# Performance work log

Hardware: AMD Instinct MI355X
Metric: run time of the kernel (lower is better)

Reference implementation:

```python
import jax, jax.numpy as jnp
import numpy as np
from jax import lax


def setup_inputs() -> dict:
    key = jax.random.key(0)
    B, N, R = 16, 4096, 256
    param = jax.random.normal(key, (B, N, R), dtype=jnp.float32)
    return {"param": param}


def reference(param) -> jnp.ndarray:
    # StiefelHouseholder.forward with is_thin=True (rank != n):
    #   v = tril(param, -1) + eye(n, rank)      -> unit-lower columns v_i
    #   tau_i = 2 / ||v_i||^2
    #   Q = (I - tau_1 v_1 v_1^T) ... (I - tau_R v_R v_R^T) @ I[:, :R]
    B, N, R = param.shape
    eye = jnp.eye(N, R, dtype=param.dtype)                      # [N, R]
    v = jnp.tril(param, k=-1) + eye[None]                       # [B, N, R]
    tau = 2.0 / jnp.sum(v * v, axis=1)                          # [B, R]

    Q0 = jnp.broadcast_to(eye, (B, N, R))                       # start from thin identity

    def body(Q, i):
        vi = v[:, :, i]                                          # [B, N]
        ti = tau[:, i]                                           # [B]
        w = jnp.einsum('bn,bnk->bk', vi, Q)                      # v_i^T Q
        Q = Q - (ti[:, None] * vi)[:, :, None] * w[:, None, :]   # rank-1 update
        return Q, None

    # Apply H_R first (rightmost factor), then H_{R-1}, ..., H_1.
    Q, _ = lax.scan(body, Q0, jnp.arange(R - 1, -1, -1))
    return Q                                                     # thin [B, N, R]
```

## Files before the change

kernel.cpp:

```cpp
#include <hip/hip_runtime.h>
#include <stdint.h>

#define B_ 16
#define N_ 4096
#define R_ 256

typedef short bf16x8 __attribute__((ext_vector_type(8)));
typedef float f32x4 __attribute__((ext_vector_type(4)));
typedef uint32_t u32;


__device__ __forceinline__ u32 pack_split(float x) {
  u32 u = __float_as_uint(x);
  u32 h = u & 0xffff0000u;
  float l = x - __uint_as_float(h);
  return h | (__float_as_uint(l) >> 16);
}

__device__ __forceinline__ void unpack8(const u32* w, bf16x8& hi, bf16x8& lo) {
  union { u32 u[4]; bf16x8 v; } H, L;
#pragma unroll
  for (int i = 0; i < 4; ++i) {
    u32 a = w[2 * i], b = w[2 * i + 1];
    H.u[i] = (a >> 16) | (b & 0xffff0000u);
    L.u[i] = (a & 0xffffu) | (b << 16);
  }
  hi = H.v; lo = L.v;
}

__device__ __forceinline__ void read_frag(const u32* rowbase, int row, int q2,
                                          bf16x8& hi, bf16x8& lo) {
  u32 w[8];
  const int s = row & 7;
  *(uint4*)&w[0] = *(const uint4*)(rowbase + (((q2    ) ^ s) << 2));
  *(uint4*)&w[4] = *(const uint4*)(rowbase + (((q2 + 1) ^ s) << 2));
  unpack8(w, hi, lo);
}

__device__ __forceinline__ void read_frag_f(const float* rowbase, int row, int q2,
                                            bf16x8& hi, bf16x8& lo) {
  float w[8];
  const int s = row & 7;
  *(float4*)&w[0] = *(const float4*)(rowbase + (((q2    ) ^ s) << 2));
  *(float4*)&w[4] = *(const float4*)(rowbase + (((q2 + 1) ^ s) << 2));
  union { u32 u[4]; bf16x8 v; } H, L;
#pragma unroll
  for (int i = 0; i < 4; ++i) {
    u32 a = __float_as_uint(w[2 * i]);
    u32 b = __float_as_uint(w[2 * i + 1]);
    u32 ah = a & 0xffff0000u, bh = b & 0xffff0000u;
    float la = w[2 * i]     - __uint_as_float(ah);
    float lb = w[2 * i + 1] - __uint_as_float(bh);
    H.u[i] = (a >> 16) | bh;
    L.u[i] = (__float_as_uint(la) >> 16) | (__float_as_uint(lb) & 0xffff0000u);
  }
  hi = H.v; lo = L.v;
}

__device__ __forceinline__ f32x4 mm3(bf16x8 ah, bf16x8 al, bf16x8 bh, bf16x8 bl,
                                     f32x4 c) {
  c = __builtin_amdgcn_mfma_f32_16x16x32_bf16(al, bh, c, 0, 0, 0);
  c = __builtin_amdgcn_mfma_f32_16x16x32_bf16(ah, bl, c, 0, 0, 0);
  c = __builtin_amdgcn_mfma_f32_16x16x32_bf16(ah, bh, c, 0, 0, 0);
  return c;
}

typedef __attribute__((address_space(1))) const u32* gas_p;
typedef __attribute__((address_space(3))) u32* las_p;
__device__ __forceinline__ void async_cp16(void* lds, const void* g) {
  __builtin_amdgcn_global_load_lds((gas_p)g, (las_p)lds, 16, 0, 0);
}

__global__ __launch_bounds__(256) void gram_kernel(const float* __restrict__ param,
                                                   float* __restrict__ SP) {
  const int tile = blockIdx.x, chunk = blockIdx.y, b = blockIdx.z;
  const int j0 = (tile == 2) ? 128 : 0;
  const int k0 = (tile == 0) ? 0 : 128;
  const float* __restrict__ P = param + (size_t)b * N_ * R_;

  __shared__ u32 VT[256][32];

  const int t = threadIdx.x;
  const int lane = t & 63, wv = t >> 6;
  const int wr = wv >> 1, wc = wv & 1;
  const int l15 = lane & 15, q = lane >> 4;
  const int bbase = (tile == 1) ? 128 : 0;

  f32x4 acc[4][4];
#pragma unroll
  for (int i = 0; i < 4; ++i)
#pragma unroll
    for (int j = 0; j < 4; ++j) acc[i][j] = (f32x4){0.f, 0.f, 0.f, 0.f};

  const int nb = chunk * 256;
  const int ns = (nb > k0) ? nb : k0;
  const int ne = nb + 256;

  float ld[32];

  const int ct1 = t;
  const int ct0 = t & 127;
  const int gc0 = j0 + ct0;
  const int hb  = t >> 7;

  auto do_load = [&](int n0) {
    if (tile == 1) {
#pragma unroll
      for (int ri = 0; ri < 8; ++ri)
#pragma unroll
        for (int s = 0; s < 4; ++s)
          ld[4 * ri + s] = P[(size_t)(n0 + 4 * ri + s) * R_ + ct1];
    } else {
#pragma unroll
      for (int ri = 0; ri < 4; ++ri)
#pragma unroll
        for (int s = 0; s < 4; ++s)
          ld[4 * ri + s] = P[(size_t)(n0 + 4 * (2 * ri + hb) + s) * R_ + gc0];
    }
  };

  auto do_write = [&](int n0) {
    if (tile == 1) {
#pragma unroll
      for (int ri = 0; ri < 8; ++ri) {
        u32 qw[4];
#pragma unroll
        for (int s = 0; s < 4; ++s) {
          int n = n0 + 4 * ri + s;
          float v = (n == ct1) ? 1.f : ((n > ct1) ? ld[4 * ri + s] : 0.f);
          qw[s] = pack_split(v);
        }
        *(uint4*)&VT[ct1][((ri ^ (ct1 & 7)) << 2)] = *(uint4*)qw;
      }
    } else {
#pragma unroll
      for (int ri = 0; ri < 4; ++ri) {
        int ch = 2 * ri + hb;
        u32 qw[4];
#pragma unroll
        for (int s = 0; s < 4; ++s) {
          int n = n0 + 4 * ch + s;
          float v = (n == gc0) ? 1.f : ((n > gc0) ? ld[4 * ri + s] : 0.f);
          qw[s] = pack_split(v);
        }
        *(uint4*)&VT[ct0][((ch ^ (ct0 & 7)) << 2)] = *(uint4*)qw;
      }
    }
  };

  do_load(ns);
  for (int n0 = ns; n0 < ne; n0 += 32) {
    do_write(n0);
    __syncthreads();
    if (n0 + 32 < ne) do_load(n0 + 32);

    bf16x8 Ah[4], Al[4];
#pragma unroll
    for (int mt = 0; mt < 4; ++mt) {
      int row = 64 * wr + 16 * mt + l15;
      read_frag(&VT[row][0], row, 2 * q, Ah[mt], Al[mt]);
    }
#pragma unroll
    for (int nt = 0; nt < 4; ++nt) {
      int brow = bbase + 64 * wc + 16 * nt + l15;
      bf16x8 bh, bl;
      read_frag(&VT[brow][0], brow, 2 * q, bh, bl);
#pragma unroll
      for (int mt = 0; mt < 4; ++mt)
        acc[mt][nt] = mm3(Ah[mt], Al[mt], bh, bl, acc[mt][nt]);
    }
    __syncthreads();
  }

  float* Sp = SP + (size_t)(chunk * 16 + b) * (R_ * R_);
#pragma unroll
  for (int mt = 0; mt < 4; ++mt)
#pragma unroll
    for (int nt = 0; nt < 4; ++nt) {
      int jj = j0 + 64 * wr + 16 * mt + 4 * q;
      int kk = k0 + 64 * wc + 16 * nt + l15;
#pragma unroll
      for (int r = 0; r < 4; ++r)
        Sp[(size_t)(jj + r) * R_ + kk] = acc[mt][nt][r];
    }
}

__global__ __launch_bounds__(256) void reduce_kernel(float* __restrict__ SP) {
  const int b = blockIdx.y;
  int j = blockIdx.x * 256 + threadIdx.x;
  int r, c4;
  if (j < 8192) { r = j >> 6; c4 = j & 63; }
  else { int jj = j - 8192; r = 128 + (jj >> 5); c4 = 32 + (jj & 31); }
  size_t idx = (size_t)b * 16384 + (size_t)r * 64 + c4;
  float4* sp = (float4*)SP;
  float4 a = sp[idx];
#pragma unroll
  for (int c = 1; c < 16; ++c) {
    float4 v = sp[idx + (size_t)c * 262144];
    a.x += v.x; a.y += v.y; a.z += v.z; a.w += v.w;
  }
  sp[idx] = a;
}

#define DPP_ADD(v, ctrl, rmask)                                              \
  v += __int_as_float(__builtin_amdgcn_update_dpp(                           \
      0, __float_as_int(v), ctrl, rmask, 0xf, true))

__global__ __launch_bounds__(1024) void solve_kernel(const float* __restrict__ param,
                                                     const float* __restrict__ S,
                                                     u32* __restrict__ WtP) {
  extern __shared__ float tri[];
  const int t    = threadIdx.x;
  const int lane = t & 63;
  const int wave = t >> 6;
  const int b    = blockIdx.x >> 4;
  const int jg   = blockIdx.x & 15;
  const int k    = jg + 16 * wave;
  const float* __restrict__ Sb = S + (size_t)b * R_ * R_;
  const float* __restrict__ Pb = param + (size_t)b * N_ * R_;

  float4 x = *(const float4*)(Pb + (size_t)k * R_ + 4 * lane);
  {
    int c0 = 4 * lane;
    x.x = (c0     == k) ? 1.f : ((c0     < k) ? x.x : 0.f);
    x.y = (c0 + 1 == k) ? 1.f : ((c0 + 1 < k) ? x.y : 0.f);
    x.z = (c0 + 2 == k) ? 1.f : ((c0 + 2 < k) ? x.z : 0.f);
    x.w = (c0 + 3 == k) ? 1.f : ((c0 + 3 < k) ? x.w : 0.f);
  }

  const float4* S4 = (const float4*)Sb;
#pragma unroll
  for (int m = 0; m < 16; ++m) {
    int idx = t + 1024 * m;
    int r  = idx >> 6;
    int c4 = idx & 63;
    int g  = r >> 2;
    if (c4 >= g) {
      float4 v = S4[idx];
      int rowlen = 256 - 4 * g;
      int addr = 1024 * g - 8 * g * (g - 1) + (r & 3) * rowlen + 4 * (c4 - g);
      *(float4*)&tri[addr] = v;
    }
  }
  __syncthreads();

  float4 w = make_float4(0.f, 0.f, 0.f, 0.f);
  const int k4 = k >> 2;
  int rowlen = 256 - 4 * k4;
  int base   = 1024 * k4 - 8 * k4 * (k4 - 1);

  {
    const float* rb = tri + base + 4 * lane - 4 * k4;
    float4 rA0 = *(const float4*)(rb);
    float4 rA1 = *(const float4*)(rb + rowlen);
    float4 rA2 = *(const float4*)(rb + 2 * rowlen);
    float4 rA3 = *(const float4*)(rb + 3 * rowlen);

    for (int r4 = k4;; --r4) {
      const bool more = (r4 > 0);

      float s0 = fmaf(rA0.x, w.x, fmaf(rA0.y, w.y, fmaf(rA0.z, w.z, rA0.w * w.w)));
      float s1 = fmaf(rA1.x, w.x, fmaf(rA1.y, w.y, fmaf(rA1.z, w.z, rA1.w * w.w)));
      float s2 = fmaf(rA2.x, w.x, fmaf(rA2.y, w.y, fmaf(rA2.z, w.z, rA2.w * w.w)));
      float s3 = fmaf(rA3.x, w.x, fmaf(rA3.y, w.y, fmaf(rA3.z, w.z, rA3.w * w.w)));

      float4 rB0, rB1, rB2, rB3;
      int nrl = rowlen, nbs = base;
      if (more) {
        nrl = rowlen + 4;
        nbs = base - 4 * nrl;
        const float* rbn = tri + nbs + 4 * lane - 4 * (r4 - 1);
        rB0 = *(const float4*)(rbn);
        rB1 = *(const float4*)(rbn + nrl);
        rB2 = *(const float4*)(rbn + 2 * nrl);
        rB3 = *(const float4*)(rbn + 3 * nrl);
      }
      __builtin_amdgcn_sched_barrier(0);

      DPP_ADD(s0, 0x111, 0xf); DPP_ADD(s1, 0x111, 0xf);
      DPP_ADD(s2, 0x111, 0xf); DPP_ADD(s3, 0x111, 0xf);
      DPP_ADD(s0, 0x112, 0xf); DPP_ADD(s1, 0x112, 0xf);
      DPP_ADD(s2, 0x112, 0xf); DPP_ADD(s3, 0x112, 0xf);
      DPP_ADD(s0, 0x114, 0xf); DPP_ADD(s1, 0x114, 0xf);
      DPP_ADD(s2, 0x114, 0xf); DPP_ADD(s3, 0x114, 0xf);
      DPP_ADD(s0, 0x118, 0xf); DPP_ADD(s1, 0x118, 0xf);
      DPP_ADD(s2, 0x118, 0xf); DPP_ADD(s3, 0x118, 0xf);
      DPP_ADD(s0, 0x142, 0xa); DPP_ADD(s1, 0x142, 0xa);
      DPP_ADD(s2, 0x142, 0xa); DPP_ADD(s3, 0x142, 0xa);
      DPP_ADD(s0, 0x143, 0xc); DPP_ADD(s1, 0x143, 0xc);
      DPP_ADD(s2, 0x143, 0xc); DPP_ADD(s3, 0x143, 0xc);
      s0 = __int_as_float(__builtin_amdgcn_readlane(__float_as_int(s0), 63));
      s1 = __int_as_float(__builtin_amdgcn_readlane(__float_as_int(s1), 63));
      s2 = __int_as_float(__builtin_amdgcn_readlane(__float_as_int(s2), 63));
      s3 = __int_as_float(__builtin_amdgcn_readlane(__float_as_int(s3), 63));

      float w3 = 2.f * __builtin_amdgcn_rcpf(rA3.w) * (x.w - s3);
      float s2c = fmaf(rA2.w, w3, s2);
      float w2 = 2.f * __builtin_amdgcn_rcpf(rA2.z) * (x.z - s2c);
      float s1c = fmaf(rA1.z, w2, fmaf(rA1.w, w3, s1));
      float w1 = 2.f * __builtin_amdgcn_rcpf(rA1.y) * (x.y - s1c);
      float s0c = fmaf(rA0.y, w1, fmaf(rA0.z, w2, fmaf(rA0.w, w3, s0)));
      float w0 = 2.f * __builtin_amdgcn_rcpf(rA0.x) * (x.x - s0c);
      if (lane == r4) { w.w = w3; w.z = w2; w.y = w1; w.x = w0; }

      if (!more) break;
      rowlen = nrl; base = nbs;
      rA0 = rB0; rA1 = rB1; rA2 = rB2; rA3 = rB3;
    }
  }

  u32 pw[4] = { pack_split(w.x), pack_split(w.y), pack_split(w.z), pack_split(w.w) };
  *(uint4*)(WtP + ((size_t)b * R_ + k) * R_ + 4 * lane) = *(uint4*)pw;
}

__global__ __launch_bounds__(256) void final_kernel(const float* __restrict__ param,
                                                    const u32* __restrict__ WtP,
                                                    float* __restrict__ Q) {
  const int b  = blockIdx.z;
  const int n0 = blockIdx.x * 128;
  const int k0 = blockIdx.y * 128;
  const float* __restrict__ Pb = param + (size_t)b * N_ * R_;
  const u32* __restrict__ Wb = WtP + (size_t)b * R_ * R_;
  float* __restrict__ Qb = Q + (size_t)b * N_ * R_;

  __shared__ float VAf[128][32];
  __shared__ u32   WBp[128][32];

  const int t = threadIdx.x;
  const int lane = t & 63, wv = t >> 6;
  const int wr = wv >> 1, wc = wv & 1;
  const int l15 = lane & 15, q = lane >> 4;
  const int rsub = lane >> 3;
  const int csub = lane & 7;
  const int chsw = csub ^ rsub;

  f32x4 acc[4][4];
#pragma unroll
  for (int i = 0; i < 4; ++i)
#pragma unroll
    for (int j = 0; j < 4; ++j) acc[i][j] = (f32x4){0.f, 0.f, 0.f, 0.f};

  auto issue = [&](int jb) {
#pragma unroll
    for (int c = 0; c < 4; ++c) {
      int rbase = 32 * c + 8 * wv;
      int row   = rbase + rsub;
      async_cp16(&VAf[rbase][0], &Pb[(size_t)(n0 + row) * R_ + jb + 4 * chsw]);
      async_cp16(&WBp[rbase][0], &Wb[(size_t)(k0 + row) * R_ + jb + 4 * chsw]);
    }
  };

  const int jend = k0 + 128;
  issue(0);
  for (int jb = 0; jb < jend; jb += 32) {
    __syncthreads();

    if (n0 < 256 && n0 <= jb + 31) {
#pragma unroll
      for (int m = 0; m < 16; ++m) {
        int idx = t + 256 * m;
        int row = idx >> 5;
        int j   = idx & 31;
        int n   = n0 + row;
        int gj  = jb + j;
        if (n <= gj)
          VAf[row][(((j >> 2) ^ (row & 7)) << 2) + (j & 3)] = (n == gj) ? 1.f : 0.f;
      }
      __syncthreads();
    }

    bf16x8 Ah[4], Al[4], Bh[4], Bl[4];
#pragma unroll
    for (int mt = 0; mt < 4; ++mt) {
      int row = 64 * wr + 16 * mt + l15;
      read_frag_f(&VAf[row][0], row, 2 * q, Ah[mt], Al[mt]);
    }
#pragma unroll
    for (int nt = 0; nt < 4; ++nt) {
      int krow = 64 * wc + 16 * nt + l15;
      read_frag(&WBp[krow][0], krow, 2 * q, Bh[nt], Bl[nt]);
    }
    __syncthreads();

    if (jb + 32 < jend) issue(jb + 32);

#pragma unroll
    for (int nt = 0; nt < 4; ++nt)
#pragma unroll
      for (int mt = 0; mt < 4; ++mt)
        acc[mt][nt] = mm3(Ah[mt], Al[mt], Bh[nt], Bl[nt], acc[mt][nt]);
  }

  float* Ep = (float*)&VAf[0][0];
  const int erow = t >> 3;
  const int ec16 = (t & 7) * 16;
#pragma unroll
  for (int mt = 0; mt < 4; ++mt) {
    __syncthreads();
#pragma unroll
    for (int nt = 0; nt < 4; ++nt) {
      int kcol = k0 + 64 * wc + 16 * nt + l15;
#pragma unroll
      for (int r = 0; r < 4; ++r) {
        int nrow = n0 + 64 * wr + 16 * mt + 4 * q + r;
        int lrow = 16 * wr + 4 * q + r;
        Ep[lrow * 132 + 64 * wc + 16 * nt + l15] =
            ((nrow == kcol) ? 1.f : 0.f) - acc[mt][nt][r];
      }
    }
    __syncthreads();
    int grow = n0 + 64 * (erow >> 4) + 16 * mt + (erow & 15);
#pragma unroll
    for (int s = 0; s < 4; ++s) {
      float4 v = *(const float4*)&Ep[erow * 132 + ec16 + 4 * s];
      *(float4*)&Qb[(size_t)grow * R_ + k0 + ec16 + 4 * s] = v;
    }
  }
}

extern "C" void kernel_launch(void* const* d_in, const int* in_sizes, int n_in,
                              void* d_out, int out_size, void* d_ws, size_t ws_size,
                              hipStream_t stream) {
  const float* param = (const float*)d_in[0];
  float* Q  = (float*)d_out;
  float* SP = Q;
  float* S  = Q;
  u32*   WtP = (u32*)d_ws;

  gram_kernel<<<dim3(3, 16, B_), 256, 0, stream>>>(param, SP);
  reduce_kernel<<<dim3(48, 16), 256, 0, stream>>>(SP);
  solve_kernel<<<dim3(256), 1024, 133120, stream>>>(param, S, WtP);
  final_kernel<<<dim3(32, 2, B_), 256, 0, stream>>>(param, WtP, Q);
}
```

Measured before the change: 138.2 us.

## Double-buffer final_kernel shared tiles with two-stage async prefetch

Turns the shared-memory tiles in final_kernel into two ping-pong buffers and issues loads two K-steps ahead. Barriers now use explicit vmcnt and lgkmcnt waits so global loads overlap the MFMA work of the current step. The price is doubled LDS use, which may cut occupancy. At the tail it also issues redundant loads that are clamped to the last tile.

New measurement: 139.9 us. Within noise of the previous version (+1.2%).

```diff
diff --git a/kernel.cpp b/kernel.cpp
--- a/kernel.cpp
+++ b/kernel.cpp
@@ -323,8 +323,8 @@
   const u32* __restrict__ Wb = WtP + (size_t)b * R_ * R_;
   float* __restrict__ Qb = Q + (size_t)b * N_ * R_;
 
-  __shared__ float VAf[128][32];
-  __shared__ u32   WBp[128][32];
+  __shared__ float VA2[2][128][32];
+  __shared__ u32   WB2[2][128][32];
 
   const int t = threadIdx.x;
   const int lane = t & 63, wv = t >> 6;
@@ -340,20 +340,26 @@
 #pragma unroll
     for (int j = 0; j < 4; ++j) acc[i][j] = (f32x4){0.f, 0.f, 0.f, 0.f};
 
-  auto issue = [&](int jb) {
+  auto issue = [&](int jb, int p) {
 #pragma unroll
     for (int c = 0; c < 4; ++c) {
       int rbase = 32 * c + 8 * wv;
       int row   = rbase + rsub;
-      async_cp16(&VAf[rbase][0], &Pb[(size_t)(n0 + row) * R_ + jb + 4 * chsw]);
-      async_cp16(&WBp[rbase][0], &Wb[(size_t)(k0 + row) * R_ + jb + 4 * chsw]);
+      async_cp16(&VA2[p][rbase][0], &Pb[(size_t)(n0 + row) * R_ + jb + 4 * chsw]);
+      async_cp16(&WB2[p][rbase][0], &Wb[(size_t)(k0 + row) * R_ + jb + 4 * chsw]);
     }
   };
 
   const int jend = k0 + 128;
-  issue(0);
+  const int last = jend - 32;
+  issue(0, 0);
+  issue(32, 1);
   for (int jb = 0; jb < jend; jb += 32) {
-    __syncthreads();
+    const int p = (jb >> 5) & 1;
+
+    asm volatile("s_waitcnt vmcnt(8)" ::: "memory");
+    __builtin_amdgcn_s_barrier();
+    __builtin_amdgcn_sched_barrier(0);
 
     if (n0 < 256 && n0 <= jb + 31) {
 #pragma unroll
@@ -364,25 +370,31 @@
         int n   = n0 + row;
         int gj  = jb + j;
         if (n <= gj)
-          VAf[row][(((j >> 2) ^ (row & 7)) << 2) + (j & 3)] = (n == gj) ? 1.f : 0.f;
+          VA2[p][row][(((j >> 2) ^ (row & 7)) << 2) + (j & 3)] = (n == gj) ? 1.f : 0.f;
       }
-      __syncthreads();
+      asm volatile("s_waitcnt lgkmcnt(0)" ::: "memory");
+      __builtin_amdgcn_s_barrier();
+      __builtin_amdgcn_sched_barrier(0);
     }
 
     bf16x8 Ah[4], Al[4], Bh[4], Bl[4];
 #pragma unroll
     for (int mt = 0; mt < 4; ++mt) {
       int row = 64 * wr + 16 * mt + l15;
-      read_frag_f(&VAf[row][0], row, 2 * q, Ah[mt], Al[mt]);
+      read_frag_f(&VA2[p][row][0], row, 2 * q, Ah[mt], Al[mt]);
     }
 #pragma unroll
     for (int nt = 0; nt < 4; ++nt) {
       int krow = 64 * wc + 16 * nt + l15;
-      read_frag(&WBp[krow][0], krow, 2 * q, Bh[nt], Bl[nt]);
-    }
-    __syncthreads();
-
-    if (jb + 32 < jend) issue(jb + 32);
+      read_frag(&WB2[p][krow][0], krow, 2 * q, Bh[nt], Bl[nt]);
+    }
+
+    asm volatile("s_waitcnt lgkmcnt(0)" ::: "memory");
+    __builtin_amdgcn_s_barrier();
+    __builtin_amdgcn_sched_barrier(0);
+
+    int jn = jb + 64; if (jn > last) jn = last;
+    issue(jn, p);
 
 #pragma unroll
     for (int nt = 0; nt < 4; ++nt)
@@ -391,7 +403,10 @@
         acc[mt][nt] = mm3(Ah[mt], Al[mt], Bh[nt], Bl[nt], acc[mt][nt]);
   }
 
-  float* Ep = (float*)&VAf[0][0];
+  asm volatile("s_waitcnt vmcnt(0)" ::: "memory");
+  __syncthreads();
+
+  float* Ep = (float*)&VA2[0][0][0];
   const int erow = t >> 3;
   const int ec16 = (t & 7) * 16;
 #pragma unroll
```

## Store W factor as single rounded bf16 and drop lo term in final GEMM

Applied to the files above, without the earlier changes.

The solve kernel now writes the W matrix as round-to-nearest bf16 only (half the bytes) instead of a hi/lo split pair. The final GEMM loads a half-size W tile with a new swizzle and runs two MFMAs per tile (A_hi and A_lo against W_hi) instead of three. The heavier k-half block is also scheduled first. This cuts workspace traffic, LDS use and MFMA count, but loses the low-order part of W, which risks accuracy against the fp32 reference.

After: 133.6 us. -3.4%, faster.

```diff
diff --git a/kernel.cpp b/kernel.cpp
--- a/kernel.cpp
+++ b/kernel.cpp
@@ -9,6 +9,11 @@
 typedef float f32x4 __attribute__((ext_vector_type(4)));
 typedef uint32_t u32;
 
+
+__device__ __forceinline__ u32 rne16(float x) {
+  u32 u = __float_as_uint(x);
+  return (u + 0x7fffu + ((u >> 16) & 1u)) >> 16;
+}
 
 __device__ __forceinline__ u32 pack_split(float x) {
   u32 u = __float_as_uint(x);
@@ -208,7 +213,7 @@
 
 __global__ __launch_bounds__(1024) void solve_kernel(const float* __restrict__ param,
                                                      const float* __restrict__ S,
-                                                     u32* __restrict__ WtP) {
+                                                     u32* __restrict__ Whg) {
   extern __shared__ float tri[];
   const int t    = threadIdx.x;
   const int lane = t & 63;
@@ -309,22 +314,25 @@
     }
   }
 
-  u32 pw[4] = { pack_split(w.x), pack_split(w.y), pack_split(w.z), pack_split(w.w) };
-  *(uint4*)(WtP + ((size_t)b * R_ + k) * R_ + 4 * lane) = *(uint4*)pw;
+  u32 p0 = rne16(w.x) | (rne16(w.y) << 16);
+  u32 p1 = rne16(w.z) | (rne16(w.w) << 16);
+  *(uint2*)(Whg + ((size_t)b * R_ + k) * 128 + 2 * lane) = make_uint2(p0, p1);
 }
 
 __global__ __launch_bounds__(256) void final_kernel(const float* __restrict__ param,
-                                                    const u32* __restrict__ WtP,
+                                                    const u32* __restrict__ Whg,
                                                     float* __restrict__ Q) {
   const int b  = blockIdx.z;
   const int n0 = blockIdx.x * 128;
-  const int k0 = blockIdx.y * 128;
+  const int k0 = (blockIdx.y == 0) ? 128 : 0;
   const float* __restrict__ Pb = param + (size_t)b * N_ * R_;
-  const u32* __restrict__ Wb = WtP + (size_t)b * R_ * R_;
+  const u32* __restrict__ Wb = Whg + (size_t)b * R_ * 128;
   float* __restrict__ Qb = Q + (size_t)b * N_ * R_;
 
-  __shared__ float VAf[128][32];
-  __shared__ u32   WBp[128][32];
+  __shared__ struct {
+    float VAf[128][32];
+    u32   WBh[128][16];
+  } sm;
 
   const int t = threadIdx.x;
   const int lane = t & 63, wv = t >> 6;
@@ -332,7 +340,8 @@
   const int l15 = lane & 15, q = lane >> 4;
   const int rsub = lane >> 3;
   const int csub = lane & 7;
-  const int chsw = csub ^ rsub;
+  const int wrow4 = lane >> 2;
+  const int wch   = lane & 3;
 
   f32x4 acc[4][4];
 #pragma unroll
@@ -345,8 +354,16 @@
     for (int c = 0; c < 4; ++c) {
       int rbase = 32 * c + 8 * wv;
       int row   = rbase + rsub;
-      async_cp16(&VAf[rbase][0], &Pb[(size_t)(n0 + row) * R_ + jb + 4 * chsw]);
-      async_cp16(&WBp[rbase][0], &Wb[(size_t)(k0 + row) * R_ + jb + 4 * chsw]);
+      async_cp16(&sm.VAf[rbase][0],
+                 &Pb[(size_t)(n0 + row) * R_ + jb + 4 * (csub ^ (row & 7))]);
+    }
+#pragma unroll
+    for (int c = 0; c < 2; ++c) {
+      int rbase = 16 * (wv + 4 * c);
+      int row   = rbase + wrow4;
+      async_cp16(&sm.WBh[rbase][0],
+                 &Wb[(size_t)(k0 + row) * 128 + (jb >> 1) +
+                     4 * (wch ^ ((row >> 1) & 3))]);
     }
   };
 
@@ -364,21 +381,23 @@
         int n   = n0 + row;
         int gj  = jb + j;
         if (n <= gj)
-          VAf[row][(((j >> 2) ^ (row & 7)) << 2) + (j & 3)] = (n == gj) ? 1.f : 0.f;
+          sm.VAf[row][(((j >> 2) ^ (row & 7)) << 2) + (j & 3)] = (n == gj) ? 1.f : 0.f;
       }
       __syncthreads();
     }
 
-    bf16x8 Ah[4], Al[4], Bh[4], Bl[4];
+    bf16x8 Ah[4], Al[4], Bh[4];
 #pragma unroll
     for (int mt = 0; mt < 4; ++mt) {
       int row = 64 * wr + 16 * mt + l15;
-      read_frag_f(&VAf[row][0], row, 2 * q, Ah[mt], Al[mt]);
+      read_frag_f(&sm.VAf[row][0], row, 2 * q, Ah[mt], Al[mt]);
     }
 #pragma unroll
     for (int nt = 0; nt < 4; ++nt) {
       int krow = 64 * wc + 16 * nt + l15;
-      read_frag(&WBp[krow][0], krow, 2 * q, Bh[nt], Bl[nt]);
+      union { uint4 u; bf16x8 v; } X;
+      X.u = *(const uint4*)(&sm.WBh[krow][(q ^ ((krow >> 1) & 3)) << 2]);
+      Bh[nt] = X.v;
     }
     __syncthreads();
 
@@ -387,11 +406,17 @@
 #pragma unroll
     for (int nt = 0; nt < 4; ++nt)
 #pragma unroll
-      for (int mt = 0; mt < 4; ++mt)
-        acc[mt][nt] = mm3(Ah[mt], Al[mt], Bh[nt], Bl[nt], acc[mt][nt]);
-  }
-
-  float* Ep = (float*)&VAf[0][0];
+      for (int mt = 0; mt < 4; ++mt) {
+        acc[mt][nt] = __builtin_amdgcn_mfma_f32_16x16x32_bf16(
+            Al[mt], Bh[nt], acc[mt][nt], 0, 0, 0);
+        acc[mt][nt] = __builtin_amdgcn_mfma_f32_16x16x32_bf16(
+            Ah[mt], Bh[nt], acc[mt][nt], 0, 0, 0);
+      }
+  }
+
+  __syncthreads();
+
+  float* Ep = (float*)&sm;
   const int erow = t >> 3;
   const int ec16 = (t & 7) * 16;
 #pragma unroll
@@ -425,10 +450,10 @@
   float* Q  = (float*)d_out;
   float* SP = Q;
   float* S  = Q;
-  u32*   WtP = (u32*)d_ws;
+  u32*   Whg = (u32*)d_ws;
 
   gram_kernel<<<dim3(3, 16, B_), 256, 0, stream>>>(param, SP);
   reduce_kernel<<<dim3(48, 16), 256, 0, stream>>>(SP);
-  solve_kernel<<<dim3(256), 1024, 133120, stream>>>(param, S, WtP);
-  final_kernel<<<dim3(32, 2, B_), 256, 0, stream>>>(param, WtP, Q);
-}
+  solve_kernel<<<dim3(256), 1024, 133120, stream>>>(param, S, Whg);
+  final_kernel<<<dim3(32, 2, B_), 256, 0, stream>>>(param, Whg, Q);
+}
```
